# Kernel tuning notes

Hardware: AMD Instinct MI355X
Metric: run time of the kernel (lower is better)

The kernel has to match this reference:

```python
import jax, jax.numpy as jnp
import numpy as np

U_NODES, V_NODES, N_EDGES = 100000, 50000, 2000000
F_DIM, G_DIM, H_DIM = 32, 32, 8
G_HIDDEN = (64, 32)
F_HIDDEN = (64, 32)
OUT_DIM = 1


def _linear_params(key, din, dout):
    kw, kb = jax.random.split(key)
    lim = 1.0 / np.sqrt(din)
    w = jax.random.uniform(kw, (din, dout), jnp.float32, -lim, lim)
    b = jax.random.uniform(kb, (dout,), jnp.float32, -lim, lim)
    return w, b


def setup_inputs() -> dict:
    key = jax.random.key(0)
    ks = jax.random.split(key, 10)
    u = jax.random.normal(ks[0], (U_NODES, F_DIM), jnp.float32)
    v = jax.random.normal(ks[1], (V_NODES, G_DIM), jnp.float32)
    e_vals = jax.random.normal(ks[2], (N_EDGES, H_DIM), jnp.float32)
    e_src = jax.random.randint(ks[3], (N_EDGES,), 0, V_NODES, jnp.int32)  # V-side index (indices[0])
    e_dst = jax.random.randint(ks[4], (N_EDGES,), 0, U_NODES, jnp.int32)  # U-side index (indices[1])
    g_w1, g_b1 = _linear_params(ks[5], F_DIM + G_DIM + H_DIM, G_HIDDEN[0])
    g_w2, g_b2 = _linear_params(ks[6], G_HIDDEN[0], G_HIDDEN[1])
    f_w1, f_b1 = _linear_params(ks[7], F_DIM + G_HIDDEN[1], F_HIDDEN[0])
    f_w2, f_b2 = _linear_params(ks[8], F_HIDDEN[0], F_HIDDEN[1])
    t_w, t_b = _linear_params(ks[9], F_HIDDEN[1], OUT_DIM)
    return {
        "u": u, "v": v, "e_vals": e_vals, "e_src": e_src, "e_dst": e_dst,
        "g_w1": g_w1, "g_b1": g_b1, "g_w2": g_w2, "g_b2": g_b2,
        "f_w1": f_w1, "f_b1": f_b1, "f_w2": f_w2, "f_b2": f_b2,
        "t_w": t_w, "t_b": t_b,
    }


def reference(u, v, e_vals, e_src, e_dst,
              g_w1, g_b1, g_w2, g_b2,
              f_w1, f_b1, f_w2, f_b2,
              t_w, t_b):
    # gather edge endpoint features -> g MLP (two Linear+ReLU layers)
    edge_in = jnp.concatenate([u[e_dst], v[e_src], e_vals], axis=-1)  # (E, F+G+H)
    h = jax.nn.relu(edge_in @ g_w1 + g_b1)
    h = jax.nn.relu(h @ g_w2 + g_b2)  # (E, D)
    # torch.sparse.sum over dim=-3 (V axis) == segment-sum by the U index
    agg = jax.ops.segment_sum(h, e_dst, num_segments=u.shape[0])  # (U, D)
    # f MLP on concat([u, agg])
    z = jax.nn.relu(jnp.concatenate([u, agg], axis=-1) @ f_w1 + f_b1)
    z = jax.nn.relu(z @ f_w2 + f_b2)
    # tail linear (no relu) + sigmoid
    return jax.nn.sigmoid(z @ t_w + t_b)  # (U, 1)
```

## Files before the change

kernel.cpp:

```cpp
#include <hip/hip_runtime.h>
#include <cstdint>
#include <cstddef>

#define U_NODES 100000
#define V_NODES 50000
#define N_EDGES 2000000
#define UBLKS ((U_NODES + 255) / 256)
#define VBLKS ((V_NODES + 255) / 256)

#define BNODES 64
#define NBUK ((U_NODES + BNODES - 1) / BNODES)
#define SCAP_PT 7
#define SCAP (SCAP_PT * 256)
#define DFLAG 0x10000000


typedef _Float16 f16x8 __attribute__((ext_vector_type(8)));
typedef _Float16 f16x2 __attribute__((ext_vector_type(2)));
typedef float    f32x4 __attribute__((ext_vector_type(4)));

__device__ __forceinline__ void load8f(const float* __restrict__ p, float* x) {
    const float4* p4 = reinterpret_cast<const float4*>(p);
    float4 a = p4[0], b = p4[1];
    x[0]=a.x; x[1]=a.y; x[2]=a.z; x[3]=a.w;
    x[4]=b.x; x[5]=b.y; x[6]=b.z; x[7]=b.w;
}

__device__ __forceinline__ void load32f(const float* __restrict__ p, float* x) {
    #pragma unroll
    for (int q = 0; q < 4; ++q) load8f(p + 8*q, x + 8*q);
}

__device__ __forceinline__ unsigned pack_bf16x2(float a, float b) {
    unsigned ua = __float_as_uint(a);
    ua = (ua + 0x7FFFu + ((ua >> 16) & 1u)) >> 16;
    unsigned ub = __float_as_uint(b);
    ub = (ub + 0x7FFFu + ((ub >> 16) & 1u)) & 0xFFFF0000u;
    return ua | ub;
}
__device__ __forceinline__ unsigned short bf16_1(float a) {
    unsigned ua = __float_as_uint(a);
    return (unsigned short)((ua + 0x7FFFu + ((ua >> 16) & 1u)) >> 16);
}

__device__ __forceinline__ unsigned pk16(float a, float b) {
    union { f16x2 h; unsigned u; } c;
    c.h[0] = (_Float16)a; c.h[1] = (_Float16)b;
    return c.u;
}
__device__ __forceinline__ float f16lo(unsigned w) {
    union { unsigned short u; _Float16 h; } c; c.u = (unsigned short)(w & 0xFFFFu);
    return (float)c.h;
}
__device__ __forceinline__ float f16hi(unsigned w) {
    union { unsigned short u; _Float16 h; } c; c.u = (unsigned short)(w >> 16);
    return (float)c.h;
}
__device__ __forceinline__ f16x8 as_f16x8(uint4 x) {
    union { uint4 u; f16x8 h; } c; c.u = x; return c.h;
}

__device__ __forceinline__ float fdot2f(unsigned a, unsigned b, float c) {
#if defined(__has_builtin) && __has_builtin(__builtin_amdgcn_fdot2)
    union { unsigned u; f16x2 h; } ca, cb; ca.u = a; cb.u = b;
    return __builtin_amdgcn_fdot2(ca.h, cb.h, c, false);
#else
    return c + f16lo(a)*f16lo(b) + f16hi(a)*f16hi(b);
#endif
}


__global__ __launch_bounds__(256) void proj_u_kernel(
    const float* __restrict__ u, const float* __restrict__ g_w1,
    float* __restrict__ A)
{
    int n = blockIdx.x * 256 + threadIdx.x;
    if (n >= U_NODES) return;
    float x[32];
    load32f(u + (size_t)n * 32, x);
    float acc[64];
    #pragma unroll
    for (int j = 0; j < 64; ++j) acc[j] = 0.f;
    #pragma unroll
    for (int i = 0; i < 32; ++i) {
        #pragma unroll
        for (int j = 0; j < 64; ++j) acc[j] += x[i] * g_w1[i*64 + j];
    }
    float4* Ap = reinterpret_cast<float4*>(A + (size_t)n * 64);
    #pragma unroll
    for (int q = 0; q < 16; ++q)
        Ap[q] = make_float4(acc[4*q], acc[4*q+1], acc[4*q+2], acc[4*q+3]);
}

__global__ __launch_bounds__(256) void proj_v_kernel(
    const float* __restrict__ v, const float* __restrict__ g_w1,
    const float* __restrict__ g_b1, float* __restrict__ B)
{
    int n = blockIdx.x * 256 + threadIdx.x;
    if (n >= V_NODES) return;
    float x[32];
    load32f(v + (size_t)n * 32, x);
    float acc[64];
    #pragma unroll
    for (int j = 0; j < 64; ++j) acc[j] = g_b1[j];
    #pragma unroll
    for (int i = 0; i < 32; ++i) {
        #pragma unroll
        for (int j = 0; j < 64; ++j) acc[j] += x[i] * g_w1[(32+i)*64 + j];
    }
    float4* Bp = reinterpret_cast<float4*>(B + (size_t)n * 64);
    #pragma unroll
    for (int q = 0; q < 16; ++q)
        Bp[q] = make_float4(acc[4*q], acc[4*q+1], acc[4*q+2], acc[4*q+3]);
}


__global__ __launch_bounds__(1024) void bucket_hist_kernel(
    const int* __restrict__ e_dst, int* __restrict__ bucketcnt,
    int* __restrict__ blockbase, int epb)
{
    __shared__ int hist[NBUK];
    const int tid = threadIdx.x, blk = blockIdx.x;
    for (int i = tid; i < NBUK; i += 1024) hist[i] = 0;
    __syncthreads();
    int e0 = blk * epb;
    int e1 = e0 + epb; if (e1 > N_EDGES) e1 = N_EDGES;
    for (int e = e0 + tid; e < e1; e += 1024)
        atomicAdd(&hist[e_dst[e] >> 6], 1);
    __syncthreads();
    for (int b = tid; b < NBUK; b += 1024) {
        int c = hist[b];
        blockbase[blk * NBUK + b] = c ? atomicAdd(&bucketcnt[b], c) : 0;
    }
}

__global__ __launch_bounds__(256) void scan_block_kernel(
    const int* __restrict__ deg, int* __restrict__ off, int* __restrict__ aux, int n)
{
    __shared__ int s[256];
    int tid = threadIdx.x;
    int i = blockIdx.x * 256 + tid;
    int x = (i < n) ? deg[i] : 0;
    s[tid] = x;
    __syncthreads();
    #pragma unroll
    for (int o = 1; o < 256; o <<= 1) {
        int t = (tid >= o) ? s[tid - o] : 0;
        __syncthreads();
        s[tid] += t;
        __syncthreads();
    }
    if (i < n) off[i + 1] = s[tid];
    if (tid == 255) aux[blockIdx.x] = s[255];
}

__global__ __launch_bounds__(512) void scan_aux_kernel(int* __restrict__ aux, int nA)
{
    __shared__ int s[512];
    int tid = threadIdx.x;
    int x = (tid < nA) ? aux[tid] : 0;
    s[tid] = x;
    __syncthreads();
    #pragma unroll
    for (int o = 1; o < 512; o <<= 1) {
        int t = (tid >= o) ? s[tid - o] : 0;
        __syncthreads();
        s[tid] += t;
        __syncthreads();
    }
    if (tid < nA) aux[tid] = s[tid] - x;
}

__global__ __launch_bounds__(256) void scan_add_kernel(
    int* __restrict__ off, const int* __restrict__ aux, int n)
{
    int i = blockIdx.x * 256 + threadIdx.x;
    if (i == 0) off[0] = 0;
    if (i < n) off[i + 1] += aux[i >> 8];
}

__global__ __launch_bounds__(1024) void bucket_pack_kernel(
    const int* __restrict__ e_dst, const int* __restrict__ e_src,
    const float* __restrict__ e_vals, const int* __restrict__ bucket_off,
    const int* __restrict__ blockbase, unsigned* __restrict__ epk, int epb)
{
    __shared__ int cur[NBUK];
    __shared__ int base[NBUK];
    const int tid = threadIdx.x, blk = blockIdx.x;
    for (int i = tid; i < NBUK; i += 1024) {
        cur[i] = 0;
        base[i] = bucket_off[i] + blockbase[blk * NBUK + i];
    }
    __syncthreads();
    int e0 = blk * epb;
    int e1 = e0 + epb; if (e1 > N_EDGES) e1 = N_EDGES;
    for (int e = e0 + tid; e < e1; e += 1024) {
        int d = e_dst[e];
        int b = d >> 6;
        int lr = atomicAdd(&cur[b], 1);
        int pos = base[b] + lr;
        float ev[8];
        load8f(e_vals + (size_t)e * 8, ev);
        uint4 w0;
        w0.x = (unsigned)d;
        w0.y = (unsigned)e_src[e];
        w0.z = pk16(ev[0], ev[1]);
        w0.w = pk16(ev[2], ev[3]);
        uint2 w1;
        w1.x = pk16(ev[4], ev[5]);
        w1.y = pk16(ev[6], ev[7]);
        unsigned* dst = epk + (size_t)pos * 8;
        *reinterpret_cast<uint4*>(dst)     = w0;
        *reinterpret_cast<uint2*>(dst + 4) = w1;
    }
}

__global__ __launch_bounds__(256) void sort_bucket_kernel(
    unsigned* __restrict__ epk, const int* __restrict__ bucket_off)
{
    __shared__ int h[BNODES];
    __shared__ int basec[BNODES];
    const int tid = threadIdx.x, bk = blockIdx.x;
    const int beg = bucket_off[bk];
    const int cnt = bucket_off[bk + 1] - beg;
    if (cnt <= 0) return;
    if (cnt > SCAP) {
        for (int i = tid; i < cnt; i += 256)
            epk[(size_t)(beg + i) * 8] |= DFLAG;
        return;
    }
    if (tid < BNODES) h[tid] = 0;
    __syncthreads();

    uint4 rA[SCAP_PT]; uint2 rB[SCAP_PT];
    #pragma unroll
    for (int k = 0; k < SCAP_PT; ++k) {
        int i = tid + k * 256;
        if (i < cnt) {
            const unsigned* ep = epk + (size_t)(beg + i) * 8;
            rA[k] = *reinterpret_cast<const uint4*>(ep);
            rB[k] = *reinterpret_cast<const uint2*>(ep + 4);
            atomicAdd(&h[rA[k].x & (BNODES - 1)], 1);
        }
    }
    __syncthreads();
    if (tid == 0) {
        int run = 0;
        #pragma unroll
        for (int j = 0; j < BNODES; ++j) { basec[j] = run; run += h[j]; }
    }
    __syncthreads();
    if (tid < BNODES) h[tid] = 0;
    __syncthreads();
    #pragma unroll
    for (int k = 0; k < SCAP_PT; ++k) {
        int i = tid + k * 256;
        if (i < cnt) {
            int d6 = rA[k].x & (BNODES - 1);
            int p = basec[d6] + atomicAdd(&h[d6], 1);
            unsigned* dst = epk + (size_t)(beg + p) * 8;
            *reinterpret_cast<uint4*>(dst)     = rA[k];
            *reinterpret_cast<uint2*>(dst + 4) = rB[k];
        }
    }
}


__global__ __launch_bounds__(256) void edge_frag_kernel(
    const float* __restrict__ A, const float* __restrict__ B,
    const unsigned* __restrict__ epk,
    const float* __restrict__ g_w1, const float* __restrict__ g_w2,
    const float* __restrict__ g_b2, float* __restrict__ agg)
{
    __shared__ unsigned s_w2[32 * 33];
    __shared__ __align__(16) unsigned s_w1e[4 * 64];
    __shared__ unsigned s_h2[256 * 17];
    __shared__ int s_d[256];
    __shared__ int s_heads[256];
    __shared__ int s_cnt, s_prevd, s_nextd;

    const int tid = threadIdx.x;
    const long bP = (long)blockIdx.x * 256;

    #pragma unroll
    for (int i = 0; i < 4; ++i) {
        int idx = tid + i * 256;
        int kp = idx >> 5, n = idx & 31;
        s_w2[kp * 33 + n] = pk16(g_w2[(2*kp)*32 + n], g_w2[(2*kp+1)*32 + n]);
    }
    {
        int i2 = tid >> 6, c = tid & 63;
        s_w1e[i2 * 64 + c] = pk16(g_w1[(64 + 2*i2)*64 + c], g_w1[(64 + 2*i2 + 1)*64 + c]);
    }
    if (tid == 0) {
        s_cnt = 0;
        s_prevd = (bP > 0) ? (int)epk[(size_t)(bP - 1) * 8] : -2;
        s_nextd = (bP + 256 < (long)N_EDGES) ? (int)epk[(size_t)(bP + 256) * 8] : -2;
    }

    const int wv   = tid >> 6;
    const int lane = tid & 63;
    const int lm   = lane & 15;
    const int lg   = lane >> 4;
    const long wP  = bP + wv * 64;

    int dM[4], sM[4];
    unsigned evp[4][4];
    #pragma unroll
    for (int mt = 0; mt < 4; ++mt) {
        long pe = wP + mt*16 + lm;
        if (pe < (long)N_EDGES) {
            const unsigned* ep = epk + (size_t)pe * 8;
            uint4 w0 = *reinterpret_cast<const uint4*>(ep);
            uint2 w1 = *reinterpret_cast<const uint2*>(ep + 4);
            dM[mt] = (int)w0.x; sM[mt] = (int)w0.y;
            evp[mt][0] = w0.z; evp[mt][1] = w0.w; evp[mt][2] = w1.x; evp[mt][3] = w1.y;
        } else {
            dM[mt] = -1; sM[mt] = 0;
            evp[mt][0] = evp[mt][1] = evp[mt][2] = evp[mt][3] = 0;
        }
        if (lg == 0) s_d[wv*64 + mt*16 + lm] = dM[mt];
    }
    __syncthreads();

    if (bP + tid < (long)N_EDGES) {
        int d_me  = s_d[tid];
        int prevd = (tid == 0) ? s_prevd : s_d[tid - 1];
        bool true_head = (prevd != d_me);
        bool is_head = (tid == 0) || true_head;
        if (is_head) {
            int idx = atomicAdd(&s_cnt, 1);
            s_heads[idx] = tid | (true_head ? 0x10000 : 0);
        }
    }

    uint4 afr[4][2];
    #pragma unroll
    for (int kt = 0; kt < 2; ++kt) {
        float acc[4][8];
        #pragma unroll
        for (int mt = 0; mt < 4; ++mt) {
            if (dM[mt] >= 0) {
                size_t dn = (size_t)(dM[mt] & 0x0FFFFFFF);
                const float4* Ap = reinterpret_cast<const float4*>(A + dn*64 + kt*32 + lg*8);
                const float4* Bp = reinterpret_cast<const float4*>(B + (size_t)sM[mt]*64 + kt*32 + lg*8);
                float4 a0 = Ap[0], a1 = Ap[1], b0 = Bp[0], b1 = Bp[1];
                acc[mt][0] = a0.x + b0.x; acc[mt][1] = a0.y + b0.y;
                acc[mt][2] = a0.z + b0.z; acc[mt][3] = a0.w + b0.w;
                acc[mt][4] = a1.x + b1.x; acc[mt][5] = a1.y + b1.y;
                acc[mt][6] = a1.z + b1.z; acc[mt][7] = a1.w + b1.w;
            } else {
                #pragma unroll
                for (int j = 0; j < 8; ++j) acc[mt][j] = 0.f;
            }
        }
        #pragma unroll
        for (int i2 = 0; i2 < 4; ++i2) {
            uint4 wA = *reinterpret_cast<const uint4*>(&s_w1e[i2*64 + kt*32 + lg*8]);
            uint4 wB = *reinterpret_cast<const uint4*>(&s_w1e[i2*64 + kt*32 + lg*8 + 4]);
            #pragma unroll
            for (int mt = 0; mt < 4; ++mt) {
                unsigned e2 = evp[mt][i2];
                acc[mt][0] = fdot2f(e2, wA.x, acc[mt][0]);
                acc[mt][1] = fdot2f(e2, wA.y, acc[mt][1]);
                acc[mt][2] = fdot2f(e2, wA.z, acc[mt][2]);
                acc[mt][3] = fdot2f(e2, wA.w, acc[mt][3]);
                acc[mt][4] = fdot2f(e2, wB.x, acc[mt][4]);
                acc[mt][5] = fdot2f(e2, wB.y, acc[mt][5]);
                acc[mt][6] = fdot2f(e2, wB.z, acc[mt][6]);
                acc[mt][7] = fdot2f(e2, wB.w, acc[mt][7]);
            }
        }
        #pragma unroll
        for (int mt = 0; mt < 4; ++mt) {
            uint4 w;
            w.x = pk16(fmaxf(acc[mt][0], 0.f), fmaxf(acc[mt][1], 0.f));
            w.y = pk16(fmaxf(acc[mt][2], 0.f), fmaxf(acc[mt][3], 0.f));
            w.z = pk16(fmaxf(acc[mt][4], 0.f), fmaxf(acc[mt][5], 0.f));
            w.w = pk16(fmaxf(acc[mt][6], 0.f), fmaxf(acc[mt][7], 0.f));
            afr[mt][kt] = w;
        }
    }

    f32x4 mac[4][2];
    #pragma unroll
    for (int mt = 0; mt < 4; ++mt) {
        #pragma unroll
        for (int nt = 0; nt < 2; ++nt) {
            mac[mt][nt][0] = 0.f; mac[mt][nt][1] = 0.f;
            mac[mt][nt][2] = 0.f; mac[mt][nt][3] = 0.f;
        }
    }
    #pragma unroll
    for (int kt = 0; kt < 2; ++kt) {
        uint4 bf0, bf1;
        int kp = kt*16 + lg*4;
        bf0.x = s_w2[(kp+0)*33 + lm];      bf1.x = s_w2[(kp+0)*33 + 16 + lm];
        bf0.y = s_w2[(kp+1)*33 + lm];      bf1.y = s_w2[(kp+1)*33 + 16 + lm];
        bf0.z = s_w2[(kp+2)*33 + lm];      bf1.z = s_w2[(kp+2)*33 + 16 + lm];
        bf0.w = s_w2[(kp+3)*33 + lm];      bf1.w = s_w2[(kp+3)*33 + 16 + lm];
        f16x8 b0 = as_f16x8(bf0), b1 = as_f16x8(bf1);
        #pragma unroll
        for (int mt = 0; mt < 4; ++mt) {
            f16x8 a = as_f16x8(afr[mt][kt]);
            mac[mt][0] = __builtin_amdgcn_mfma_f32_16x16x32_f16(a, b0, mac[mt][0], 0, 0, 0);
            mac[mt][1] = __builtin_amdgcn_mfma_f32_16x16x32_f16(a, b1, mac[mt][1], 0, 0, 0);
        }
    }

    float b2a = g_b2[lm], b2b = g_b2[16 + lm];
    unsigned short* h2s = reinterpret_cast<unsigned short*>(s_h2);
    #pragma unroll
    for (int mt = 0; mt < 4; ++mt) {
        #pragma unroll
        for (int r = 0; r < 4; ++r) {
            int edge = wv*64 + mt*16 + lg*4 + r;
            h2s[edge*34 + lm]      = bf16_1(fmaxf(mac[mt][0][r] + b2a, 0.f));
            h2s[edge*34 + 16 + lm] = bf16_1(fmaxf(mac[mt][1][r] + b2b, 0.f));
        }
    }
    __syncthreads();

    const int nseg = s_cnt;
    const int next_d = s_nextd;
    for (int w = tid; w < nseg * 16; w += 256) {
        int seg = w >> 4, cp = w & 15;
        int ent = s_heads[seg];
        int h = ent & 0xFFFF;
        bool thead = (ent & 0x10000) != 0;
        int dd = s_d[h];
        float s0 = 0.f, s1 = 0.f;
        int r = h;
        while (r < 256 && s_d[r] == dd) {
            unsigned x = s_h2[r*17 + cp];
            s0 += __uint_as_float(x << 16);
            s1 += __uint_as_float(x & 0xFFFF0000u);
            ++r;
        }
        bool end_complete = (r < 256) || (next_d != dd);
        int node = dd & 0x0FFFFFFF;
        bool flg = (dd & DFLAG) != 0;
        float* dst = agg + (size_t)node * 32 + 2 * cp;
        if (thead && end_complete && !flg) {
            *reinterpret_cast<float2*>(dst) = make_float2(s0, s1);
        } else {
            atomicAdd(dst + 0, s0);
            atomicAdd(dst + 1, s1);
        }
    }
}


__global__ __launch_bounds__(256) void node_kernel(
    const float* __restrict__ u, const float* __restrict__ agg,
    const float* __restrict__ f_w1, const float* __restrict__ f_b1,
    const float* __restrict__ f_w2, const float* __restrict__ f_b2,
    const float* __restrict__ t_w, const float* __restrict__ t_b,
    float* __restrict__ out)
{
    int n = blockIdx.x * 256 + threadIdx.x;
    if (n >= U_NODES) return;
    float x[64];
    load32f(u   + (size_t)n * 32, x);
    load32f(agg + (size_t)n * 32, x + 32);
    float z1[64];
    #pragma unroll
    for (int j = 0; j < 64; ++j) z1[j] = f_b1[j];
    #pragma unroll
    for (int i = 0; i < 64; ++i) {
        #pragma unroll
        for (int j = 0; j < 64; ++j) z1[j] += x[i] * f_w1[i*64 + j];
    }
    #pragma unroll
    for (int j = 0; j < 64; ++j) z1[j] = fmaxf(z1[j], 0.f);
    float z2[32];
    #pragma unroll
    for (int k = 0; k < 32; ++k) z2[k] = f_b2[k];
    #pragma unroll
    for (int j = 0; j < 64; ++j) {
        #pragma unroll
        for (int k = 0; k < 32; ++k) z2[k] += z1[j] * f_w2[j*32 + k];
    }
    #pragma unroll
    for (int k = 0; k < 32; ++k) z2[k] = fmaxf(z2[k], 0.f);
    float o = t_b[0];
    #pragma unroll
    for (int k = 0; k < 32; ++k) o += z2[k] * t_w[k];
    out[n] = 1.f / (1.f + expf(-o));
}


__global__ __launch_bounds__(256) void rank_kernel(
    const int* __restrict__ e_dst, int* __restrict__ deg, int* __restrict__ rank)
{
    int e = blockIdx.x * 256 + threadIdx.x;
    if (e >= N_EDGES) return;
    rank[e] = atomicAdd(&deg[e_dst[e]], 1);
}

__global__ __launch_bounds__(256) void scatter_kernel(
    const int* __restrict__ e_dst, const int* __restrict__ off,
    const int* __restrict__ rank, int* __restrict__ sorted_eid)
{
    int e = blockIdx.x * 256 + threadIdx.x;
    if (e >= N_EDGES) return;
    int d = e_dst[e];
    sorted_eid[off[d] + rank[e]] = e;
}

template <bool HAS_A, bool HAS_B>
__global__ __launch_bounds__(256) void edge_sorted_kernel(
    const float* __restrict__ A, const float* __restrict__ B,
    const float* __restrict__ u, const float* __restrict__ v,
    const float* __restrict__ e_vals, const int* __restrict__ e_src,
    const int* __restrict__ e_dst, const int* __restrict__ seid,
    const float* __restrict__ g_w1, const float* __restrict__ g_b1,
    const float* __restrict__ g_w2, const float* __restrict__ g_b2,
    float* __restrict__ agg)
{
    __shared__ unsigned lds_h[256][17];
    __shared__ int lds_d[256];
    __shared__ int lds_heads[256];
    __shared__ int lds_cnt;
    __shared__ int lds_prev_d, lds_next_d;

    const int tid = threadIdx.x;
    const long p = (long)blockIdx.x * 256 + tid;

    if (tid == 0) {
        lds_cnt = 0;
        long pprev = (long)blockIdx.x * 256 - 1;
        lds_prev_d = (pprev < 0) ? -2 : e_dst[seid[pprev]];
        long pnext = (long)blockIdx.x * 256 + 256;
        lds_next_d = (pnext >= N_EDGES) ? -2 : e_dst[seid[pnext]];
    }

    int d = -1;
    if (p < N_EDGES) {
        int eid = seid[p];
        d = e_dst[eid];
        int s = e_src[eid];

        float h1[64];
        if constexpr (HAS_A) {
            const float4* Ap = reinterpret_cast<const float4*>(A + (size_t)d * 64);
            #pragma unroll
            for (int q = 0; q < 16; ++q) {
                float4 a = Ap[q];
                h1[4*q+0] = a.x; h1[4*q+1] = a.y; h1[4*q+2] = a.z; h1[4*q+3] = a.w;
            }
        } else {
            #pragma unroll
            for (int j = 0; j < 64; ++j) h1[j] = 0.f;
            float x[32];
            load32f(u + (size_t)d * 32, x);
            #pragma unroll
            for (int i = 0; i < 32; ++i) {
                #pragma unroll
                for (int j = 0; j < 64; ++j) h1[j] += x[i] * g_w1[i*64 + j];
            }
        }
        if constexpr (HAS_B) {
            const float4* Bp = reinterpret_cast<const float4*>(B + (size_t)s * 64);
            #pragma unroll
            for (int q = 0; q < 16; ++q) {
                float4 b = Bp[q];
                h1[4*q+0] += b.x; h1[4*q+1] += b.y; h1[4*q+2] += b.z; h1[4*q+3] += b.w;
            }
        } else {
            #pragma unroll
            for (int j = 0; j < 64; ++j) h1[j] += g_b1[j];
            float x[32];
            load32f(v + (size_t)s * 32, x);
            #pragma unroll
            for (int i = 0; i < 32; ++i) {
                #pragma unroll
                for (int j = 0; j < 64; ++j) h1[j] += x[i] * g_w1[(32+i)*64 + j];
            }
        }
        float ev[8];
        load8f(e_vals + (size_t)eid * 8, ev);
        #pragma unroll
        for (int i = 0; i < 8; ++i) {
            #pragma unroll
            for (int j = 0; j < 64; ++j) h1[j] += ev[i] * g_w1[(64+i)*64 + j];
        }
        #pragma unroll
        for (int j = 0; j < 64; ++j) h1[j] = fmaxf(h1[j], 0.f);

        float h2[32];
        #pragma unroll
        for (int k = 0; k < 32; ++k) h2[k] = g_b2[k];
        #pragma unroll
        for (int i = 0; i < 64; ++i) {
            #pragma unroll
            for (int k = 0; k < 32; ++k) h2[k] += h1[i] * g_w2[i*32 + k];
        }
        #pragma unroll
        for (int cp = 0; cp < 16; ++cp)
            lds_h[tid][cp] = pack_bf16x2(fmaxf(h2[2*cp], 0.f), fmaxf(h2[2*cp+1], 0.f));
    }
    lds_d[tid] = d;
    __syncthreads();

    if (p < N_EDGES) {
        int prevd = (tid == 0) ? lds_prev_d : lds_d[tid - 1];
        bool true_head = (prevd != d);
        bool is_head = (tid == 0) || true_head;
        if (is_head) {
            int idx = atomicAdd(&lds_cnt, 1);
            lds_heads[idx] = tid | (true_head ? 0x10000 : 0);
        }
    }
    __syncthreads();

    const int nseg = lds_cnt;
    const int next_d = lds_next_d;
    for (int w = tid; w < nseg * 16; w += 256) {
        int seg = w >> 4, cp = w & 15;
        int ent = lds_heads[seg];
        int h = ent & 0xFFFF;
        bool thead = (ent & 0x10000) != 0;
        int dd = lds_d[h];
        float s0 = 0.f, s1 = 0.f;
        int r = h;
        while (r < 256 && lds_d[r] == dd) {
            unsigned x = lds_h[r][cp];
            s0 += __uint_as_float(x << 16);
            s1 += __uint_as_float(x & 0xFFFF0000u);
            ++r;
        }
        bool end_complete = (r < 256) || (next_d != dd);
        float* dst = agg + (size_t)dd * 32 + 2 * cp;
        if (thead && end_complete) {
            *reinterpret_cast<float2*>(dst) = make_float2(s0, s1);
        } else {
            atomicAdd(dst + 0, s0);
            atomicAdd(dst + 1, s1);
        }
    }
}

__global__ __launch_bounds__(256) void edge_direct_kernel(
    const float* __restrict__ u, const float* __restrict__ v,
    const float* __restrict__ e_vals, const int* __restrict__ e_src,
    const int* __restrict__ e_dst, const float* __restrict__ g_w1,
    const float* __restrict__ g_b1, const float* __restrict__ g_w2,
    const float* __restrict__ g_b2, float* __restrict__ agg)
{
    int e = blockIdx.x * 256 + threadIdx.x;
    if (e >= N_EDGES) return;
    int d = e_dst[e];
    int s = e_src[e];
    float x[72];
    load32f(u + (size_t)d * 32, x);
    load32f(v + (size_t)s * 32, x + 32);
    load8f(e_vals + (size_t)e * 8, x + 64);
    float h1[64];
    #pragma unroll
    for (int j = 0; j < 64; ++j) h1[j] = g_b1[j];
    #pragma unroll
    for (int i = 0; i < 72; ++i) {
        #pragma unroll
        for (int j = 0; j < 64; ++j) h1[j] += x[i] * g_w1[i*64 + j];
    }
    #pragma unroll
    for (int j = 0; j < 64; ++j) h1[j] = fmaxf(h1[j], 0.f);
    float acc2[32];
    #pragma unroll
    for (int k = 0; k < 32; ++k) acc2[k] = g_b2[k];
    #pragma unroll
    for (int i = 0; i < 64; ++i) {
        #pragma unroll
        for (int k = 0; k < 32; ++k) acc2[k] += h1[i] * g_w2[i*32 + k];
    }
    float* aggp = agg + (size_t)d * 32;
    #pragma unroll
    for (int k = 0; k < 32; ++k) atomicAdd(aggp + k, fmaxf(acc2[k], 0.f));
}


static inline size_t align256(size_t x) { return (x + 255) & ~(size_t)255; }

extern "C" void kernel_launch(void* const* d_in, const int* in_sizes, int n_in,
                              void* d_out, int out_size, void* d_ws, size_t ws_size,
                              hipStream_t stream) {
    const float* u      = (const float*)d_in[0];
    const float* v      = (const float*)d_in[1];
    const float* e_vals = (const float*)d_in[2];
    const int*   e_src  = (const int*)  d_in[3];
    const int*   e_dst  = (const int*)  d_in[4];
    const float* g_w1   = (const float*)d_in[5];
    const float* g_b1   = (const float*)d_in[6];
    const float* g_w2   = (const float*)d_in[7];
    const float* g_b2   = (const float*)d_in[8];
    const float* f_w1   = (const float*)d_in[9];
    const float* f_b1   = (const float*)d_in[10];
    const float* f_w2   = (const float*)d_in[11];
    const float* f_b2   = (const float*)d_in[12];
    const float* t_w    = (const float*)d_in[13];
    const float* t_b    = (const float*)d_in[14];
    float* out = (float*)d_out;

    char* wsc = (char*)d_ws;
    const int eBlocks = (N_EDGES + 255) / 256;
    const int nChunksB = (NBUK + 255) / 256;

    const size_t bcB   = align256((size_t)NBUK * 4);
    const size_t boB   = align256((size_t)(NBUK + 1) * 4);
    const size_t auxB  = align256((size_t)nChunksB * 4);
    const size_t aggB  = align256((size_t)U_NODES * 32 * 4);
    const size_t epkB  = align256((size_t)N_EDGES * 32);
    const size_t bB    = align256((size_t)V_NODES * 64 * 4);
    const size_t aB    = align256((size_t)U_NODES * 64 * 4);
    const size_t e4B   = align256((size_t)N_EDGES * 4);

    auto layoutNeed = [&](int hb, size_t* offs) -> size_t {
        size_t bbB = align256((size_t)hb * NBUK * 4);
        size_t o = 0;
        offs[0] = o; o += bcB;
        offs[1] = o; o += boB;
        offs[2] = o; o += auxB;
        offs[3] = o; o += bbB;
        offs[4] = o; o += aggB;
        offs[5] = o; o += epkB;
        offs[6] = o; o += bB;
        offs[7] = o; o += aB;
        return o;
    };
    size_t offs256[8], offs128[8];
    size_t need256 = layoutNeed(256, offs256);
    size_t need128 = layoutNeed(128, offs128);

    const size_t degB = align256((size_t)U_NODES * 4);
    const size_t offB = align256((size_t)(U_NODES + 1) * 4);
    const int nChunksU = (U_NODES + 255) / 256;
    const size_t auxUB = align256((size_t)nChunksU * 4);
    size_t o3 = 0;
    size_t oDeg3 = o3; o3 += degB;
    size_t oOff3 = o3; o3 += offB;
    size_t oAux3 = o3; o3 += auxUB;
    size_t oAgg3 = o3; o3 += aggB;
    size_t oSeid = o3; o3 += e4B;
    size_t needT4 = o3 + e4B;
    size_t oB3 = o3;   o3 += bB;
    size_t oA3 = o3;   o3 += aB;
    size_t needT3 = o3;

    if (ws_size >= need128) {
        const int HBn = (ws_size >= need256) ? 256 : 128;
        const size_t* of = (ws_size >= need256) ? offs256 : offs128;
        const int epb = (N_EDGES + HBn - 1) / HBn;

        int* bucketcnt = (int*)(wsc + of[0]);
        int* bucketoff = (int*)(wsc + of[1]);
        int* aux       = (int*)(wsc + of[2]);
        int* blockbase = (int*)(wsc + of[3]);
        float* agg     = (float*)(wsc + of[4]);
        unsigned* epk  = (unsigned*)(wsc + of[5]);
        float* B       = (float*)(wsc + of[6]);
        float* A       = (float*)(wsc + of[7]);

        hipMemsetAsync(bucketcnt, 0, (size_t)NBUK * 4, stream);
        hipMemsetAsync(agg, 0, (size_t)U_NODES * 32 * 4, stream);

        bucket_hist_kernel<<<HBn, 1024, 0, stream>>>(e_dst, bucketcnt, blockbase, epb);
        scan_block_kernel<<<nChunksB, 256, 0, stream>>>(bucketcnt, bucketoff, aux, NBUK);
        scan_aux_kernel<<<1, 512, 0, stream>>>(aux, nChunksB);
        scan_add_kernel<<<nChunksB, 256, 0, stream>>>(bucketoff, aux, NBUK);
        bucket_pack_kernel<<<HBn, 1024, 0, stream>>>(e_dst, e_src, e_vals,
                                                     bucketoff, blockbase, epk, epb);
        sort_bucket_kernel<<<NBUK, 256, 0, stream>>>(epk, bucketoff);
        proj_v_kernel<<<VBLKS, 256, 0, stream>>>(v, g_w1, g_b1, B);
        proj_u_kernel<<<UBLKS, 256, 0, stream>>>(u, g_w1, A);
        edge_frag_kernel<<<eBlocks, 256, 0, stream>>>(A, B, epk, g_w1, g_w2, g_b2, agg);
        node_kernel<<<UBLKS, 256, 0, stream>>>(
            u, agg, f_w1, f_b1, f_w2, f_b2, t_w, t_b, out);
    } else if (ws_size >= needT4) {
        const bool hasAB = (ws_size >= needT3);
        int* deg   = (int*)(wsc + oDeg3);
        int* off   = (int*)(wsc + oOff3);
        int* aux   = (int*)(wsc + oAux3);
        float* agg = (float*)(wsc + oAgg3);
        int* seid  = (int*)(wsc + oSeid);
        float* B = hasAB ? (float*)(wsc + oB3) : nullptr;
        float* A = hasAB ? (float*)(wsc + oA3) : nullptr;
        int* rank = hasAB ? (int*)A : (int*)(wsc + oSeid + e4B);

        hipMemsetAsync(deg, 0, (size_t)U_NODES * 4, stream);
        hipMemsetAsync(agg, 0, (size_t)U_NODES * 32 * 4, stream);

        rank_kernel<<<eBlocks, 256, 0, stream>>>(e_dst, deg, rank);
        scan_block_kernel<<<nChunksU, 256, 0, stream>>>(deg, off, aux, U_NODES);
        scan_aux_kernel<<<1, 512, 0, stream>>>(aux, nChunksU);
        scan_add_kernel<<<nChunksU, 256, 0, stream>>>(off, aux, U_NODES);
        scatter_kernel<<<eBlocks, 256, 0, stream>>>(e_dst, off, rank, seid);

        if (hasAB) {
            proj_v_kernel<<<VBLKS, 256, 0, stream>>>(v, g_w1, g_b1, B);
            proj_u_kernel<<<UBLKS, 256, 0, stream>>>(u, g_w1, A);
            edge_sorted_kernel<true, true><<<eBlocks, 256, 0, stream>>>(
                A, B, u, v, e_vals, e_src, e_dst, seid, g_w1, g_b1, g_w2, g_b2, agg);
        } else {
            edge_sorted_kernel<false, false><<<eBlocks, 256, 0, stream>>>(
                nullptr, nullptr, u, v, e_vals, e_src, e_dst, seid,
                g_w1, g_b1, g_w2, g_b2, agg);
        }
        node_kernel<<<UBLKS, 256, 0, stream>>>(
            u, agg, f_w1, f_b1, f_w2, f_b2, t_w, t_b, out);
    } else {
        float* agg0 = (float*)wsc;
        hipMemsetAsync(agg0, 0, (size_t)U_NODES * 32 * 4, stream);
        edge_direct_kernel<<<eBlocks, 256, 0, stream>>>(
            u, v, e_vals, e_src, e_dst, g_w1, g_b1, g_w2, g_b2, agg0);
        node_kernel<<<UBLKS, 256, 0, stream>>>(
            u, agg0, f_w1, f_b1, f_w2, f_b2, t_w, t_b, out);
    }
}
```

Measured before the change: 405.0 us.

## Sort compact (dst, edge id) keys, then gather edge payload once

The bucket pass now scatters only 8-byte (dst, edge id) keys instead of full 32-byte packed edge records. The per-bucket sort orders these keys in shared memory and gathers e_src and e_vals by edge id, writing each packed record to its final position once. This replaces a 32-byte scatter plus a 32-byte read and rewrite of every record with a smaller key scatter and reread. The cost is random gathers of e_vals and e_src in the sort kernel, since they are no longer read in edge order. The key buffer shares workspace with A, which is written only after the sort finishes.

```diff
diff --git a/kernel.cpp b/kernel.cpp
--- a/kernel.cpp
+++ b/kernel.cpp
@@ -179,10 +179,9 @@
     if (i < n) off[i + 1] += aux[i >> 8];
 }
 
-__global__ __launch_bounds__(1024) void bucket_pack_kernel(
-    const int* __restrict__ e_dst, const int* __restrict__ e_src,
-    const float* __restrict__ e_vals, const int* __restrict__ bucket_off,
-    const int* __restrict__ blockbase, unsigned* __restrict__ epk, int epb)
+__global__ __launch_bounds__(1024) void pack_keys_kernel(
+    const int* __restrict__ e_dst, const int* __restrict__ bucket_off,
+    const int* __restrict__ blockbase, uint2* __restrict__ keys, int epb)
 {
     __shared__ int cur[NBUK];
     __shared__ int base[NBUK];
@@ -198,49 +197,54 @@
         int d = e_dst[e];
         int b = d >> 6;
         int lr = atomicAdd(&cur[b], 1);
-        int pos = base[b] + lr;
-        float ev[8];
-        load8f(e_vals + (size_t)e * 8, ev);
-        uint4 w0;
-        w0.x = (unsigned)d;
-        w0.y = (unsigned)e_src[e];
-        w0.z = pk16(ev[0], ev[1]);
-        w0.w = pk16(ev[2], ev[3]);
-        uint2 w1;
-        w1.x = pk16(ev[4], ev[5]);
-        w1.y = pk16(ev[6], ev[7]);
-        unsigned* dst = epk + (size_t)pos * 8;
-        *reinterpret_cast<uint4*>(dst)     = w0;
-        *reinterpret_cast<uint2*>(dst + 4) = w1;
-    }
-}
-
-__global__ __launch_bounds__(256) void sort_bucket_kernel(
-    unsigned* __restrict__ epk, const int* __restrict__ bucket_off)
+        keys[base[b] + lr] = make_uint2((unsigned)d, (unsigned)e);
+    }
+}
+
+__global__ __launch_bounds__(256) void sort_mat_kernel(
+    const uint2* __restrict__ keys, const int* __restrict__ bucket_off,
+    const int* __restrict__ e_src, const float* __restrict__ e_vals,
+    unsigned* __restrict__ epk)
 {
     __shared__ int h[BNODES];
     __shared__ int basec[BNODES];
+    __shared__ uint2 skey[SCAP];
     const int tid = threadIdx.x, bk = blockIdx.x;
     const int beg = bucket_off[bk];
     const int cnt = bucket_off[bk + 1] - beg;
     if (cnt <= 0) return;
+
     if (cnt > SCAP) {
-        for (int i = tid; i < cnt; i += 256)
-            epk[(size_t)(beg + i) * 8] |= DFLAG;
+        for (int i = tid; i < cnt; i += 256) {
+            uint2 key = keys[beg + i];
+            int d = (int)key.x, eid = (int)key.y;
+            float ev[8];
+            load8f(e_vals + (size_t)eid * 8, ev);
+            uint4 w0;
+            w0.x = (unsigned)(d | DFLAG);
+            w0.y = (unsigned)e_src[eid];
+            w0.z = pk16(ev[0], ev[1]);
+            w0.w = pk16(ev[2], ev[3]);
+            uint2 w1;
+            w1.x = pk16(ev[4], ev[5]);
+            w1.y = pk16(ev[6], ev[7]);
+            unsigned* dst = epk + (size_t)(beg + i) * 8;
+            *reinterpret_cast<uint4*>(dst)     = w0;
+            *reinterpret_cast<uint2*>(dst + 4) = w1;
+        }
         return;
     }
+
     if (tid < BNODES) h[tid] = 0;
     __syncthreads();
 
-    uint4 rA[SCAP_PT]; uint2 rB[SCAP_PT];
+    uint2 rK[SCAP_PT];
     #pragma unroll
     for (int k = 0; k < SCAP_PT; ++k) {
         int i = tid + k * 256;
         if (i < cnt) {
-            const unsigned* ep = epk + (size_t)(beg + i) * 8;
-            rA[k] = *reinterpret_cast<const uint4*>(ep);
-            rB[k] = *reinterpret_cast<const uint2*>(ep + 4);
-            atomicAdd(&h[rA[k].x & (BNODES - 1)], 1);
+            rK[k] = keys[beg + i];
+            atomicAdd(&h[rK[k].x & (BNODES - 1)], 1);
         }
     }
     __syncthreads();
@@ -256,11 +260,31 @@
     for (int k = 0; k < SCAP_PT; ++k) {
         int i = tid + k * 256;
         if (i < cnt) {
-            int d6 = rA[k].x & (BNODES - 1);
-            int p = basec[d6] + atomicAdd(&h[d6], 1);
-            unsigned* dst = epk + (size_t)(beg + p) * 8;
-            *reinterpret_cast<uint4*>(dst)     = rA[k];
-            *reinterpret_cast<uint2*>(dst + 4) = rB[k];
+            int d6 = rK[k].x & (BNODES - 1);
+            skey[basec[d6] + atomicAdd(&h[d6], 1)] = rK[k];
+        }
+    }
+    __syncthreads();
+
+    #pragma unroll
+    for (int k = 0; k < SCAP_PT; ++k) {
+        int i = tid + k * 256;
+        if (i < cnt) {
+            uint2 key = skey[i];
+            int d = (int)key.x, eid = (int)key.y;
+            float ev[8];
+            load8f(e_vals + (size_t)eid * 8, ev);
+            uint4 w0;
+            w0.x = (unsigned)d;
+            w0.y = (unsigned)e_src[eid];
+            w0.z = pk16(ev[0], ev[1]);
+            w0.w = pk16(ev[2], ev[3]);
+            uint2 w1;
+            w1.x = pk16(ev[4], ev[5]);
+            w1.y = pk16(ev[6], ev[7]);
+            unsigned* dst = epk + (size_t)(beg + i) * 8;
+            *reinterpret_cast<uint4*>(dst)     = w0;
+            *reinterpret_cast<uint2*>(dst + 4) = w1;
         }
     }
 }
@@ -714,6 +738,7 @@
     const size_t bB    = align256((size_t)V_NODES * 64 * 4);
     const size_t aB    = align256((size_t)U_NODES * 64 * 4);
     const size_t e4B   = align256((size_t)N_EDGES * 4);
+    const size_t keysB = align256((size_t)N_EDGES * 8);
 
     auto layoutNeed = [&](int hb, size_t* offs) -> size_t {
         size_t bbB = align256((size_t)hb * NBUK * 4);
@@ -725,7 +750,7 @@
         offs[4] = o; o += aggB;
         offs[5] = o; o += epkB;
         offs[6] = o; o += bB;
-        offs[7] = o; o += aB;
+        offs[7] = o; o += (aB > keysB ? aB : keysB);
         return o;
     };
     size_t offs256[8], offs128[8];
@@ -760,6 +785,7 @@
         unsigned* epk  = (unsigned*)(wsc + of[5]);
         float* B       = (float*)(wsc + of[6]);
         float* A       = (float*)(wsc + of[7]);
+        uint2* keys    = (uint2*)(wsc + of[7]);
 
         hipMemsetAsync(bucketcnt, 0, (size_t)NBUK * 4, stream);
         hipMemsetAsync(agg, 0, (size_t)U_NODES * 32 * 4, stream);
@@ -768,9 +794,9 @@
         scan_block_kernel<<<nChunksB, 256, 0, stream>>>(bucketcnt, bucketoff, aux, NBUK);
         scan_aux_kernel<<<1, 512, 0, stream>>>(aux, nChunksB);
         scan_add_kernel<<<nChunksB, 256, 0, stream>>>(bucketoff, aux, NBUK);
-        bucket_pack_kernel<<<HBn, 1024, 0, stream>>>(e_dst, e_src, e_vals,
-                                                     bucketoff, blockbase, epk, epb);
-        sort_bucket_kernel<<<NBUK, 256, 0, stream>>>(epk, bucketoff);
+        pack_keys_kernel<<<HBn, 1024, 0, stream>>>(e_dst, bucketoff, blockbase,
+                                                   keys, epb);
+        sort_mat_kernel<<<NBUK, 256, 0, stream>>>(keys, bucketoff, e_src, e_vals, epk);
         proj_v_kernel<<<VBLKS, 256, 0, stream>>>(v, g_w1, g_b1, B);
         proj_u_kernel<<<UBLKS, 256, 0, stream>>>(u, g_w1, A);
         edge_frag_kernel<<<eBlocks, 256, 0, stream>>>(A, B, epk, g_w1, g_w2, g_b2, agg);
```

After: 435.3 us. +7.5%, slower.
